# Optimization experiments

Hardware: AMD Instinct MI355X
Metric: run time of the kernel (lower is better)

## Reference

```python
import jax, jax.numpy as jnp
import numpy as np

N_NODES = 100000
N_PER_GRAPH = 200
N_GRAPHS = N_NODES // N_PER_GRAPH
N_EDGES = 400000
F_IN = 37
H = 128          # node_hidden == transformer_hidden == fc_hidden
HEADS = 8
K_SEEDS = 75     # ceil(0.25 * 300) -> PyG GMT defaults


def _lin(key, out_d, in_d):
    kw, kb = jax.random.split(key)
    w = jax.random.normal(kw, (out_d, in_d), jnp.float32) * float(1.0 / np.sqrt(in_d))
    b = jax.random.normal(kb, (out_d,), jnp.float32) * 0.02
    return w, b


def gcn_layer(x, W, b, src, dst, n):
    # PyG GCNConv with add_self_loops and symmetric deg^-1/2 normalization
    h = x @ W.T                                   # [n, out]
    deg = jnp.ones((n,), h.dtype).at[dst].add(1.0)   # in-degree + self loop
    dinv = jax.lax.rsqrt(deg)
    msg = h[src] * (dinv[src] * dinv[dst])[:, None]  # gather + edge normalize
    agg = jnp.zeros_like(h).at[dst].add(msg)         # scatter-add
    agg = agg + h * (dinv * dinv)[:, None]           # self-loop message
    return agg + b


def attn_block(Q, K, V, fo_W, fo_b):
    # MAB core of GMT: multi-head attention (scaled by sqrt(dim_V)) + rFF residual
    B, nq, d = Q.shape
    dh = d // HEADS
    Qh = Q.reshape(B, nq, HEADS, dh)
    Kh = K.reshape(B, K.shape[1], HEADS, dh)
    Vh = V.reshape(B, V.shape[1], HEADS, dh)
    scores = jnp.einsum('bqhd,bkhd->bhqk', Qh, Kh) / jnp.sqrt(jnp.asarray(d, Q.dtype))
    A = jax.nn.softmax(scores, axis=-1)
    O = jnp.einsum('bhqk,bkhd->bqhd', A, Vh).reshape(B, nq, d)
    out = Q + O
    return out + jax.nn.relu(out @ fo_W.T + fo_b)


def setup_inputs() -> dict:
    key = jax.random.key(0)
    k = iter(jax.random.split(key, 64))
    inp = {}
    inp['herg_em'] = jax.random.normal(next(k), (1, 1280), jnp.float32)
    inp['x'] = jax.random.normal(next(k), (N_NODES, F_IN), jnp.float32)
    inp['edge_attr'] = jax.random.normal(next(k), (N_EDGES, 4), jnp.float32)
    inp['mol_rep'] = jax.random.normal(next(k), (N_GRAPHS, 11), jnp.float32)
    for i, in_d in enumerate([F_IN, H, H, H]):
        inp[f'conv_W{i}'], inp[f'conv_b{i}'] = _lin(next(k), H, in_d)
    inp['lin1_W'], inp['lin1_b'] = _lin(next(k), H, H)
    inp['lin2_W'], inp['lin2_b'] = _lin(next(k), H, H)
    inp['S1'] = jax.random.normal(next(k), (1, K_SEEDS, H), jnp.float32) * 0.1
    for p in ['pma1', 'sab', 'pma2']:
        for nm in ['fq', 'k', 'v', 'fo']:
            inp[f'{p}_{nm}_W'], inp[f'{p}_{nm}_b'] = _lin(next(k), H, H)
    inp['S2'] = jax.random.normal(next(k), (1, 1, H), jnp.float32) * 0.1
    inp['herg_lin_W'], inp['herg_lin_b'] = _lin(next(k), H, 1280)
    inp['herg_out_W'], inp['herg_out_b'] = _lin(next(k), H, 2 * H)
    inp['fc0_W'], inp['fc0_b'] = _lin(next(k), H, H)
    inp['sig_W'], inp['sig_b'] = _lin(next(k), 1, H)
    inp['edge_index'] = jax.random.randint(next(k), (2, N_EDGES), 0, N_NODES, dtype=jnp.int32)
    inp['batch'] = jnp.arange(N_NODES, dtype=jnp.int32) // N_PER_GRAPH
    return inp


def reference(herg_em, x, edge_attr, mol_rep,
              conv_W0, conv_b0, conv_W1, conv_b1, conv_W2, conv_b2, conv_W3, conv_b3,
              lin1_W, lin1_b, lin2_W, lin2_b,
              S1, pma1_fq_W, pma1_fq_b, pma1_k_W, pma1_k_b, pma1_v_W, pma1_v_b, pma1_fo_W, pma1_fo_b,
              sab_fq_W, sab_fq_b, sab_k_W, sab_k_b, sab_v_W, sab_v_b, sab_fo_W, sab_fo_b,
              S2, pma2_fq_W, pma2_fq_b, pma2_k_W, pma2_k_b, pma2_v_W, pma2_v_b, pma2_fo_W, pma2_fo_b,
              herg_lin_W, herg_lin_b, herg_out_W, herg_out_b,
              fc0_W, fc0_b, sig_W, sig_b,
              edge_index, batch):
    src, dst = edge_index[0], edge_index[1]
    n = x.shape[0]

    # stacked GCNConv + ReLU
    h = jax.nn.relu(gcn_layer(x, conv_W0, conv_b0, src, dst, n))
    for W, b in ((conv_W1, conv_b1), (conv_W2, conv_b2), (conv_W3, conv_b3)):
        h = jax.nn.relu(gcn_layer(h, W, b, src, dst, n))

    # GraphMultisetTransformer: lin1 -> GMPool_G -> SelfAtt -> GMPool_I -> lin2
    hx = h @ lin1_W.T + lin1_b                     # [N, H]
    B = N_GRAPHS

    # GMPool_G: seeds attend to GCNConv-projected keys/values (dense per graph)
    Q = jnp.broadcast_to(S1, (B, K_SEEDS, H)) @ pma1_fq_W.T + pma1_fq_b
    K = gcn_layer(hx, pma1_k_W, pma1_k_b, src, dst, n).reshape(B, N_PER_GRAPH, H)
    V = gcn_layer(hx, pma1_v_W, pma1_v_b, src, dst, n).reshape(B, N_PER_GRAPH, H)
    xb = attn_block(Q, K, V, pma1_fo_W, pma1_fo_b)     # [B, 75, H]

    # SelfAtt (SAB)
    Q = xb @ sab_fq_W.T + sab_fq_b
    K = xb @ sab_k_W.T + sab_k_b
    V = xb @ sab_v_W.T + sab_v_b
    xb = attn_block(Q, K, V, sab_fo_W, sab_fo_b)       # [B, 75, H]

    # GMPool_I: single seed, Linear keys/values
    Q = jnp.broadcast_to(S2, (B, 1, H)) @ pma2_fq_W.T + pma2_fq_b
    K = xb @ pma2_k_W.T + pma2_k_b
    V = xb @ pma2_v_W.T + pma2_v_b
    xb = attn_block(Q, K, V, pma2_fo_W, pma2_fo_b)     # [B, 1, H]

    out = xb[:, 0, :] @ lin2_W.T + lin2_b              # [B, H]

    # hERG branch
    herg = jax.nn.relu(herg_em @ herg_lin_W.T + herg_lin_b)   # [1, 128]
    herg = jnp.broadcast_to(herg, (B, herg.shape[1]))
    out = jnp.concatenate([out, herg], axis=1)                 # [B, 256]
    out = jax.nn.relu(out @ herg_out_W.T + herg_out_b)
    out = jax.nn.relu(out @ fc0_W.T + fc0_b)                   # dropout = identity (eval)
    return jax.nn.sigmoid(out @ sig_W.T + sig_b)               # [B, 1]
```

## Files before the change

### kernel.cpp

```cpp
#include <hip/hip_runtime.h>
#include <hip/hip_bf16.h>

typedef unsigned short ushort_t;
typedef unsigned int uint_t;
typedef __attribute__((ext_vector_type(8))) short short8;
typedef __attribute__((ext_vector_type(4))) float float4v;

static constexpr int NN  = 100000;
static constexpr int NE  = 400000;
static constexpr int NB  = 500;
static constexpr int NS  = 75;
static constexpr int H   = 128;
static constexpr float SCALE = 0.08838834764831845f;

union U32 { uint_t u; float f; };
__device__ __forceinline__ float bf2f(ushort_t b){ U32 t; t.u = ((uint_t)b) << 16; return t.f; }
__device__ __forceinline__ ushort_t f2bf(float f){
    U32 t; t.f = f;
    uint_t r = t.u + 0x7fffu + ((t.u >> 16) & 1u);
    return (ushort_t)(r >> 16);
}
__device__ __forceinline__ void fma8(float* a, uint4 u, float c){
    a[0] += c * bf2f((ushort_t)(u.x & 0xffff)); a[1] += c * bf2f((ushort_t)(u.x >> 16));
    a[2] += c * bf2f((ushort_t)(u.y & 0xffff)); a[3] += c * bf2f((ushort_t)(u.y >> 16));
    a[4] += c * bf2f((ushort_t)(u.z & 0xffff)); a[5] += c * bf2f((ushort_t)(u.z >> 16));
    a[6] += c * bf2f((ushort_t)(u.w & 0xffff)); a[7] += c * bf2f((ushort_t)(u.w >> 16));
}

__global__ void k_hist(int* counts, const int* __restrict__ dst, int e){
    int i = blockIdx.x*256 + threadIdx.x;
    if (i < e) atomicAdd(&counts[dst[i]], 1);
}
__global__ __launch_bounds__(256) void k_scan1(const int* __restrict__ counts,
    int* __restrict__ row_start, int* __restrict__ blockSums,
    float* __restrict__ dinv, float* __restrict__ selfc, int n){
    __shared__ int s[256];
    int t = threadIdx.x, i = blockIdx.x*256 + t;
    int v = (i < n) ? counts[i] : 0;
    s[t] = v; __syncthreads();
    #pragma unroll
    for (int off = 1; off < 256; off <<= 1){
        int add = (t >= off) ? s[t-off] : 0;
        __syncthreads();
        s[t] += add;
        __syncthreads();
    }
    if (i < n){
        row_start[i] = s[t] - v;
        float r = rsqrtf(1.f + (float)v);
        dinv[i] = r; selfc[i] = r*r;
    }
    if (t == 255) blockSums[blockIdx.x] = s[255];
}
__global__ void k_scan3(int* __restrict__ row_start, int* __restrict__ cursor,
                        const int* __restrict__ blockOff, int n, int total){
    int i = blockIdx.x*256 + threadIdx.x;
    if (i < n){
        int v = row_start[i] + blockOff[i >> 8];
        row_start[i] = v; cursor[i] = v;
    }
    if (i == 0) row_start[n] = total;
}
__global__ void k_fillcsr(const int* __restrict__ src, const int* __restrict__ dst,
    const float* __restrict__ dinv, int* cursor,
    int* __restrict__ srcs_s, float* __restrict__ ce_s, int e){
    int i = blockIdx.x*256 + threadIdx.x;
    if (i < e){
        int d = dst[i], s = src[i];
        int p = atomicAdd(&cursor[d], 1);
        srcs_s[p] = s;
        ce_s[p] = dinv[s] * dinv[d];
    }
}

struct CvtArgs { const float* w[17]; const float* w0; const float* s1; const float* s2; const float* x37; };
static constexpr int CVT_W   = 17*16384;
static constexpr int CVT_W0  = 8192;
static constexpr int CVT_S1  = 9600;
static constexpr int CVT_S2  = 128;
static constexpr int CVT_X   = NN*64;
__global__ void k_cvt_all(CvtArgs a, ushort_t* __restrict__ wbf, ushort_t* __restrict__ w0bf,
                          ushort_t* __restrict__ s1bf, ushort_t* __restrict__ s2bf,
                          ushort_t* __restrict__ xb64, int* __restrict__ counts){
    int i = blockIdx.x*256 + threadIdx.x;
    if (i < NN) counts[i] = 0;
    if (i < CVT_W){ int idx = i >> 14, off = i & 16383; wbf[i] = f2bf(a.w[idx][off]); return; }
    i -= CVT_W;
    if (i < CVT_W0){ int r = i >> 6, c = i & 63; w0bf[i] = (c < 37) ? f2bf(a.w0[r*37 + c]) : (ushort_t)0; return; }
    i -= CVT_W0;
    if (i < CVT_S1){ s1bf[i] = f2bf(a.s1[i]); return; }
    i -= CVT_S1;
    if (i < CVT_S2){ s2bf[i] = f2bf(a.s2[i]); return; }
    i -= CVT_S2;
    if (i < CVT_X){ int r = i >> 6, c = i & 63; xb64[i] = (c < 37) ? f2bf(a.x37[(size_t)r*37 + c]) : (ushort_t)0; return; }
}

__global__ __launch_bounds__(512) void k_seedq_scan2(
    const ushort_t* __restrict__ s1bf, const ushort_t* __restrict__ s2bf,
    const ushort_t* __restrict__ W1, const float* __restrict__ bias1,
    const ushort_t* __restrict__ W2q, const float* __restrict__ bias2,
    ushort_t* __restrict__ q0, ushort_t* __restrict__ q2,
    const float* __restrict__ hem, const float* __restrict__ hlW,
    const float* __restrict__ hlb, float* __restrict__ hergv,
    const int* __restrict__ blockSums, int* __restrict__ blockOff, int nb)
{
    int blk = blockIdx.x;
    int tid  = threadIdx.x;
    if (blk == 4){
        __shared__ int s[512];
        int t = tid;
        int v = (t < nb) ? blockSums[t] : 0;
        s[t] = v; __syncthreads();
        #pragma unroll
        for (int off = 1; off < 512; off <<= 1){
            int add = (t >= off) ? s[t-off] : 0;
            __syncthreads();
            s[t] += add;
            __syncthreads();
        }
        blockOff[t] = s[t] - v;
        return;
    }
    if (blk == 3){
        __shared__ float e[1280];
        for (int i = tid; i < 1280; i += 512) e[i] = hem[i];
        __syncthreads();
        if (tid < 128){
            float acc = 0.f;
            for (int k = 0; k < 1280; ++k) acc += e[k] * hlW[(size_t)tid*1280 + k];
            hergv[tid] = fmaxf(acc + hlb[tid], 0.f);
        }
        return;
    }
    if (tid >= 256) return;
    const ushort_t* x = (blk < 2) ? s1bf : s2bf;
    const ushort_t* W = (blk < 2) ? W1 : W2q;
    const float* bias = (blk < 2) ? bias1 : bias2;
    ushort_t* out = (blk < 2) ? q0 : q2;
    int M = (blk < 2) ? NS : 1;
    int base = (blk < 2) ? blk*64 : 0;
    int wid  = tid >> 6;
    int lane = tid & 63;
    int l15  = lane & 15, quad = lane >> 4;
    int row0 = base + wid*16;
    int ar   = row0 + l15; if (ar > M-1) ar = M-1;
    const short* xr = (const short*)(x + (size_t)ar*H) + quad*8;
    float4v acc[8];
    #pragma unroll
    for (int i = 0; i < 8; ++i) acc[i] = (float4v)0.f;
    #pragma unroll
    for (int kc = 0; kc < 4; ++kc){
        short8 a = *(const short8*)(xr + kc*32);
        #pragma unroll
        for (int nt = 0; nt < 8; ++nt){
            short8 b = *(const short8*)((const short*)(W + (size_t)(nt*16 + l15)*H) + kc*32 + quad*8);
            acc[nt] = __builtin_amdgcn_mfma_f32_16x16x32_bf16(a, b, acc[nt], 0, 0, 0);
        }
    }
    #pragma unroll
    for (int nt = 0; nt < 8; ++nt){
        int c = nt*16 + l15;
        float bv = bias[c];
        #pragma unroll
        for (int reg = 0; reg < 4; ++reg){
            int r = row0 + quad*4 + reg;
            if (r >= M) continue;
            out[(size_t)r*H + c] = f2bf(acc[nt][reg] + bv);
        }
    }
}

template<int NOUT, int RELU, int STAGE2, int MINW>
__global__ __launch_bounds__(256, MINW) void k_conv_fused3(
    const ushort_t* __restrict__ x,
    const int* __restrict__ row_st, const int* __restrict__ srcs,
    const float* __restrict__ ces, const float* __restrict__ selfc,
    const ushort_t* __restrict__ W, const float* __restrict__ bias0,
    const float* __restrict__ bias1,
    const ushort_t* __restrict__ W2, const float* __restrict__ bias2,
    ushort_t* __restrict__ out0, ushort_t* __restrict__ out1)
{
    __shared__ ushort_t As[32][136];
    __shared__ ushort_t Bs[(NOUT==16)?32:1][(NOUT==16)?136:1];
    const int tid = threadIdx.x;
    const int node = tid >> 3, qq = tid & 7;
    const int g = blockIdx.x*32 + node;
    float acc[16];
    #pragma unroll
    for (int i = 0; i < 16; ++i) acc[i] = 0.f;
    if (g < NN){
        const uint4* xr = (const uint4*)(x + (size_t)g*H + qq*16);
        float sc = selfc[g];
        uint4 u0 = xr[0], u1 = xr[1];
        fma8(acc+0, u0, sc); fma8(acc+8, u1, sc);
        int e = row_st[g], e1 = row_st[g+1];
        int sA = 0, sB = 0; float cA = 0.f, cB = 0.f;
        if (e < e1){ sA = srcs[e]; cA = ces[e]; }
        if (e + 1 < e1){ sB = srcs[e+1]; cB = ces[e+1]; }
        while (e + 2 <= e1){
            int sA2 = 0, sB2 = 0; float cA2 = 0.f, cB2 = 0.f;
            if (e + 2 < e1){ sA2 = srcs[e+2]; cA2 = ces[e+2]; }
            if (e + 3 < e1){ sB2 = srcs[e+3]; cB2 = ces[e+3]; }
            const uint4* pa = (const uint4*)(x + (size_t)sA*H + qq*16);
            const uint4* pb = (const uint4*)(x + (size_t)sB*H + qq*16);
            uint4 a0 = pa[0], a1 = pa[1];
            uint4 c0 = pb[0], c1 = pb[1];
            fma8(acc+0, a0, cA); fma8(acc+8, a1, cA);
            fma8(acc+0, c0, cB); fma8(acc+8, c1, cB);
            sA = sA2; sB = sB2; cA = cA2; cB = cB2;
            e += 2;
        }
        if (e < e1){
            const uint4* pa = (const uint4*)(x + (size_t)sA*H + qq*16);
            uint4 a0 = pa[0], a1 = pa[1];
            fma8(acc+0, a0, cA); fma8(acc+8, a1, cA);
        }
    }
    {
        uint_t* dst = (uint_t*)&As[node][qq*16];
        #pragma unroll
        for (int i = 0; i < 8; ++i)
            dst[i] = (uint_t)f2bf(acc[2*i]) | ((uint_t)f2bf(acc[2*i+1]) << 16);
    }
    __syncthreads();
    const int w = tid >> 6, lane = tid & 63, l15 = lane & 15, quad = lane >> 4;
    const int rt = w & 1;
    constexpr int NT = NOUT/2;
    const int ct0 = (w >> 1) * NT;
    float4v o[NT];
    #pragma unroll
    for (int t = 0; t < NT; ++t) o[t] = (float4v)0.f;
    #pragma unroll
    for (int kc = 0; kc < 4; ++kc){
        short8 a = *(const short8*)(&As[rt*16 + l15][kc*32 + quad*8]);
        #pragma unroll
        for (int t = 0; t < NT; ++t){
            short8 bfr = *(const short8*)(W + (size_t)((ct0 + t)*16 + l15)*H + kc*32 + quad*8);
            o[t] = __builtin_amdgcn_mfma_f32_16x16x32_bf16(a, bfr, o[t], 0, 0, 0);
        }
    }
    __syncthreads();
    #pragma unroll
    for (int t = 0; t < NT; ++t){
        int cg = (ct0 + t)*16 + l15;
        #pragma unroll
        for (int r = 0; r < 4; ++r){
            float v;
            if (NOUT == 8 || cg < 128){
                v = o[t][r] + bias0[cg];
                if (RELU) v = fmaxf(v, 0.f);
                As[rt*16 + quad*4 + r][cg] = f2bf(v);
            } else {
                v = o[t][r] + bias1[cg - 128];
                if (RELU) v = fmaxf(v, 0.f);
                Bs[rt*16 + quad*4 + r][cg - 128] = f2bf(v);
            }
        }
    }
    __syncthreads();
    if (STAGE2){
        float4v o2[4];
        #pragma unroll
        for (int t = 0; t < 4; ++t) o2[t] = (float4v)0.f;
        const int ct2 = (w >> 1) * 4;
        #pragma unroll
        for (int kc = 0; kc < 4; ++kc){
            short8 a = *(const short8*)(&As[rt*16 + l15][kc*32 + quad*8]);
            #pragma unroll
            for (int t = 0; t < 4; ++t){
                short8 bfr = *(const short8*)(W2 + (size_t)((ct2 + t)*16 + l15)*H + kc*32 + quad*8);
                o2[t] = __builtin_amdgcn_mfma_f32_16x16x32_bf16(a, bfr, o2[t], 0, 0, 0);
            }
        }
        __syncthreads();
        #pragma unroll
        for (int t = 0; t < 4; ++t){
            int cg = (ct2 + t)*16 + l15;
            #pragma unroll
            for (int r = 0; r < 4; ++r)
                As[rt*16 + quad*4 + r][cg] = f2bf(o2[t][r] + bias2[cg]);
        }
        __syncthreads();
    }
    if (g < NN){
        if (NOUT == 16){
            size_t kb = ((size_t)(qq >> 1)*NN + (size_t)g)*32 + (size_t)(qq & 1)*16;
            ((uint4*)(out0 + kb))[0] = *(const uint4*)&As[node][qq*16];
            ((uint4*)(out0 + kb))[1] = *(const uint4*)&As[node][qq*16 + 8];
            ((uint4*)(out1 + kb))[0] = *(const uint4*)&Bs[node][qq*16];
            ((uint4*)(out1 + kb))[1] = *(const uint4*)&Bs[node][qq*16 + 8];
        } else {
            uint4* op = (uint4*)(out0 + (size_t)g*H + qq*16);
            const uint4* sp = (const uint4*)&As[node][qq*16];
            op[0] = sp[0]; op[1] = sp[1];
        }
    }
}

__global__ __launch_bounds__(256, 8) void k_conv0b(
    const ushort_t* __restrict__ x,
    const int* __restrict__ row_st, const int* __restrict__ srcs,
    const float* __restrict__ ces, const float* __restrict__ selfc,
    const ushort_t* __restrict__ W,
    const float* __restrict__ bias,
    ushort_t* __restrict__ out)
{
    __shared__ ushort_t As[32][136];
    const int tid = threadIdx.x;
    const int node = tid >> 3, qq = tid & 7;
    const int g = blockIdx.x*32 + node;
    float acc[8];
    #pragma unroll
    for (int i = 0; i < 8; ++i) acc[i] = 0.f;
    if (g < NN){
        const uint4* xr = (const uint4*)(x + (size_t)g*64 + qq*8);
        float sc = selfc[g];
        fma8(acc, xr[0], sc);
        int e = row_st[g], e1 = row_st[g+1];
        int sA = 0, sB = 0; float cA = 0.f, cB = 0.f;
        if (e < e1){ sA = srcs[e]; cA = ces[e]; }
        if (e + 1 < e1){ sB = srcs[e+1]; cB = ces[e+1]; }
        while (e + 2 <= e1){
            int sA2 = 0, sB2 = 0; float cA2 = 0.f, cB2 = 0.f;
            if (e + 2 < e1){ sA2 = srcs[e+2]; cA2 = ces[e+2]; }
            if (e + 3 < e1){ sB2 = srcs[e+3]; cB2 = ces[e+3]; }
            uint4 a0 = *(const uint4*)(x + (size_t)sA*64 + qq*8);
            uint4 c0 = *(const uint4*)(x + (size_t)sB*64 + qq*8);
            fma8(acc, a0, cA);
            fma8(acc, c0, cB);
            sA = sA2; sB = sB2; cA = cA2; cB = cB2;
            e += 2;
        }
        if (e < e1){
            uint4 a0 = *(const uint4*)(x + (size_t)sA*64 + qq*8);
            fma8(acc, a0, cA);
        }
    }
    {
        uint_t* dst = (uint_t*)&As[node][qq*8];
        #pragma unroll
        for (int i = 0; i < 4; ++i)
            dst[i] = (uint_t)f2bf(acc[2*i]) | ((uint_t)f2bf(acc[2*i+1]) << 16);
    }
    __syncthreads();
    const int w = tid >> 6, lane = tid & 63, l15 = lane & 15, quad = lane >> 4;
    const int rt = w & 1;
    const int ct0 = (w >> 1) * 4;
    float4v o[4];
    #pragma unroll
    for (int t = 0; t < 4; ++t) o[t] = (float4v)0.f;
    #pragma unroll
    for (int kc = 0; kc < 2; ++kc){
        short8 a = *(const short8*)(&As[rt*16 + l15][kc*32 + quad*8]);
        #pragma unroll
        for (int t = 0; t < 4; ++t){
            short8 bfr = *(const short8*)(W + (size_t)((ct0 + t)*16 + l15)*64 + kc*32 + quad*8);
            o[t] = __builtin_amdgcn_mfma_f32_16x16x32_bf16(a, bfr, o[t], 0, 0, 0);
        }
    }
    __syncthreads();
    #pragma unroll
    for (int t = 0; t < 4; ++t){
        int cg = (ct0 + t)*16 + l15;
        #pragma unroll
        for (int r = 0; r < 4; ++r)
            As[rt*16 + quad*4 + r][cg] = f2bf(fmaxf(o[t][r] + bias[cg], 0.f));
    }
    __syncthreads();
    if (g < NN){
        uint4* op = (uint4*)(out + (size_t)g*H + qq*16);
        const uint4* sp = (const uint4*)&As[node][qq*16];
        op[0] = sp[0]; op[1] = sp[1];
    }
}

struct TailArgs {
    const ushort_t* Khm; const ushort_t* Vhm;
    const ushort_t* q0;  const ushort_t* q2;
    const ushort_t* p1foW; const float* p1fob;
    const ushort_t* sfqW;  const float* sfqb;
    const ushort_t* skW;   const float* skb;
    const ushort_t* svW;   const float* svb;
    const ushort_t* sfoW;  const float* sfob;
    const ushort_t* p2kW;  const float* p2kb;
    const ushort_t* p2vW;  const float* p2vb;
    const ushort_t* p2foW; const float* p2fob;
    const ushort_t* lin2W; const float* lin2b;
    const float* hergv;
    const float* hoW; const float* hob;
    const float* fcW; const float* fcb;
    const float* sW;  const float* sb;
    float* outp;
};

__global__ __launch_bounds__(512, 4) void k_graph_tail(TailArgs a){
    __shared__ ushort_t bufA[83*136];
    __shared__ ushort_t bufB[80*136];
    __shared__ ushort_t bufC[80*136];
    __shared__ ushort_t vt4[64*104];
    const int b = blockIdx.x, tid = threadIdx.x;
    const int w = tid >> 6, lane = tid & 63, l15 = lane & 15, quad = lane >> 4;

    for (int i = tid; i < 2*16*32; i += 512){
        int hh2 = i >> 9, rr = (i >> 5) & 15, kk = 200 + (i & 31);
        bufC[(hh2*16 + rr)*232 + kk] = 0;
    }
    for (int hp = 0; hp < 4; ++hp){
        __syncthreads();
        const ushort_t* Kb = a.Khm + ((size_t)hp*NB + b)*(size_t)200*32;
        for (int idx = tid; idx < 200*8; idx += 512){
            int key = idx >> 3, p = idx & 7;
            int hh = p >> 2, dl = (p & 3)*4;
            const uint_t* src = (const uint_t*)(Kb + (size_t)key*32 + hh*16 + dl);
            uint_t* d = (uint_t*)&bufB[(hh*208 + key)*24 + dl];
            d[0] = src[0]; d[1] = src[1];
        }
        const ushort_t* Vb = a.Vhm + ((size_t)hp*NB + b)*(size_t)200*32;
        for (int idx = tid; idx < 200*8; idx += 512){
            int key = idx >> 3, p = idx & 7;
            int hh = p >> 2, dl = (p & 3)*4;
            const ushort_t* src = Vb + (size_t)key*32 + hh*16 + dl;
            bufC[(hh*16 + dl+0)*232 + key] = src[0];
            bufC[(hh*16 + dl+1)*232 + key] = src[1];
            bufC[(hh*16 + dl+2)*232 + key] = src[2];
            bufC[(hh*16 + dl+3)*232 + key] = src[3];
        }
        __syncthreads();
        for (int j = w; j < 10; j += 8){
            int hl = j / 5, qt = j % 5;
            int gh = hp*2 + hl;
            ushort_t* psw = vt4 + w*512;
            int qr = qt*16 + l15; if (qr > NS-1) qr = NS-1;
            short8 av = *(const short8*)(a.q0 + (size_t)qr*H + gh*16 + (quad & 1)*8);
            short8 zero8 = (short8)0;
            bool klow = (quad < 2);
            short8 afrag = klow ? av : zero8;
            float4v s[13];
            #pragma unroll
            for (int kt = 0; kt < 13; ++kt){
                short8 bv = *(const short8*)(&bufB[(hl*208 + kt*16 + l15)*24 + (quad & 1)*8]);
                short8 bfrag = klow ? bv : zero8;
                s[kt] = __builtin_amdgcn_mfma_f32_16x16x32_bf16(afrag, bfrag, (float4v)0.f, 0, 0, 0);
            }
            float mx[4] = {-1e30f, -1e30f, -1e30f, -1e30f};
            #pragma unroll
            for (int kt = 0; kt < 13; ++kt){
                if (kt*16 + l15 >= 200){ s[kt][0]=-1e30f; s[kt][1]=-1e30f; s[kt][2]=-1e30f; s[kt][3]=-1e30f; }
                #pragma unroll
                for (int r = 0; r < 4; ++r) mx[r] = fmaxf(mx[r], s[kt][r]);
            }
            #pragma unroll
            for (int off = 1; off < 16; off <<= 1){
                #pragma unroll
                for (int r = 0; r < 4; ++r) mx[r] = fmaxf(mx[r], __shfl_xor(mx[r], off));
            }
            float sum[4] = {0.f, 0.f, 0.f, 0.f};
            float4v o = (float4v)0.f;
            #pragma unroll
            for (int kc = 0; kc < 7; ++kc){
                #pragma unroll
                for (int t2 = 0; t2 < 2; ++t2){
                    int kt = kc*2 + t2;
                    #pragma unroll
                    for (int r = 0; r < 4; ++r){
                        float e = 0.f;
                        if (kt < 13){ e = __expf((s[kt][r] - mx[r]) * SCALE); sum[r] += e; }
                        psw[(quad*4 + r)*32 + t2*16 + l15] = f2bf(e);
                    }
                }
                short8 pa = *(const short8*)(psw + l15*32 + quad*8);
                short8 vb = *(const short8*)(&bufC[(hl*16 + l15)*232 + kc*32 + quad*8]);
                o = __builtin_amdgcn_mfma_f32_16x16x32_bf16(pa, vb, o, 0, 0, 0);
            }
            #pragma unroll
            for (int off = 1; off < 16; off <<= 1){
                #pragma unroll
                for (int r = 0; r < 4; ++r) sum[r] += __shfl_xor(sum[r], off);
            }
            #pragma unroll
            for (int r = 0; r < 4; ++r){
                int row = qt*16 + quad*4 + r;
                if (row < NS){
                    float qv = bf2f(a.q0[(size_t)row*H + gh*16 + l15]);
                    bufA[row*136 + gh*16 + l15] = f2bf(qv + o[r] / sum[r]);
                }
            }
        }
    }
    __syncthreads();

    if (w >= 5){
        for (int i = tid - 320; i < 64*104/2; i += 192) ((uint_t*)vt4)[i] = 0u;
    }
    for (int rt = w; rt < 5; rt += 8){
        float4v o[8];
        #pragma unroll
        for (int i = 0; i < 8; ++i) o[i] = (float4v)0.f;
        #pragma unroll
        for (int kc = 0; kc < 4; ++kc){
            short8 av = *(const short8*)(bufA + (rt*16 + l15)*136 + kc*32 + quad*8);
            #pragma unroll
            for (int ct = 0; ct < 8; ++ct){
                short8 bv = *(const short8*)((const short*)(a.p1foW + (size_t)(ct*16 + l15)*H) + kc*32 + quad*8);
                o[ct] = __builtin_amdgcn_mfma_f32_16x16x32_bf16(av, bv, o[ct], 0, 0, 0);
            }
        }
        #pragma unroll
        for (int ct = 0; ct < 8; ++ct){
            int c = ct*16 + l15; float bb = a.p1fob[c];
            #pragma unroll
            for (int r = 0; r < 4; ++r){
                int row = rt*16 + quad*4 + r;
                float res = bf2f(bufA[row*136 + c]);
                bufA[row*136 + c] = f2bf(fmaxf(o[ct][r] + bb, 0.f) + res);
            }
        }
    }
    __syncthreads();

    for (int job = w; job < 40; job += 8){
        int rt = job >> 3, ct = job & 7;
        float4v o = (float4v)0.f;
        #pragma unroll
        for (int kc = 0; kc < 4; ++kc){
            short8 av = *(const short8*)(bufA + (rt*16 + l15)*136 + kc*32 + quad*8);
            short8 bv = *(const short8*)((const short*)(a.sfqW + (size_t)(ct*16 + l15)*H) + kc*32 + quad*8);
            o = __builtin_amdgcn_mfma_f32_16x16x32_bf16(av, bv, o, 0, 0, 0);
        }
        int c = ct*16 + l15; float bb = a.sfqb[c];
        #pragma unroll
        for (int r = 0; r < 4; ++r)
            bufB[(rt*16 + quad*4 + r)*136 + c] = f2bf(o[r] + bb);
    }
    for (int job = w; job < 40; job += 8){
        int rt = job >> 3, ct = job & 7;
        float4v o = (float4v)0.f;
        #pragma unroll
        for (int kc = 0; kc < 4; ++kc){
            short8 av = *(const short8*)(bufA + (rt*16 + l15)*136 + kc*32 + quad*8);
            short8 bv = *(const short8*)((const short*)(a.skW + (size_t)(ct*16 + l15)*H) + kc*32 + quad*8);
            o = __builtin_amdgcn_mfma_f32_16x16x32_bf16(av, bv, o, 0, 0, 0);
        }
        int c = ct*16 + l15; float bb = a.skb[c];
        #pragma unroll
        for (int r = 0; r < 4; ++r)
            bufC[(rt*16 + quad*4 + r)*136 + c] = f2bf(o[r] + bb);
    }
    __syncthreads();

    for (int pass = 0; pass < 2; ++pass){
        int hbase = pass*4;
        for (int job = w; job < 20; job += 8){
            int rt = job >> 2, ctl = job & 3;
            int ct = hbase + ctl;
            float4v o = (float4v)0.f;
            #pragma unroll
            for (int kc = 0; kc < 4; ++kc){
                short8 av = *(const short8*)(bufA + (rt*16 + l15)*136 + kc*32 + quad*8);
                short8 bv = *(const short8*)((const short*)(a.svW + (size_t)(ct*16 + l15)*H) + kc*32 + quad*8);
                o = __builtin_amdgcn_mfma_f32_16x16x32_bf16(av, bv, o, 0, 0, 0);
            }
            int c = ct*16 + l15; float bb = a.svb[c];
            #pragma unroll
            for (int r = 0; r < 4; ++r){
                int key = rt*16 + quad*4 + r;
                if (key < NS) vt4[(ctl*16 + l15)*104 + key] = f2bf(o[r] + bb);
            }
        }
        __syncthreads();
        if (w < 4){
            ushort_t* psw = (w == 0) ? bufA + 10200 :
                            (w == 1) ? bufA + 10712 :
                            (w == 2) ? bufB + 10200 : bufC + 10200;
            int hl = w, h = hbase + w;
            short8 zero8 = (short8)0;
            bool klow = (quad < 2);
            for (int qt = 0; qt < 5; ++qt){
                short8 av = *(const short8*)(bufB + (qt*16 + l15)*136 + h*16 + (quad & 1)*8);
                short8 afrag = klow ? av : zero8;
                float4v s[5];
                #pragma unroll
                for (int kt = 0; kt < 5; ++kt){
                    short8 bv = *(const short8*)(bufC + (kt*16 + l15)*136 + h*16 + (quad & 1)*8);
                    short8 bfrag = klow ? bv : zero8;
                    s[kt] = __builtin_amdgcn_mfma_f32_16x16x32_bf16(afrag, bfrag, (float4v)0.f, 0, 0, 0);
                }
                float mx[4] = {-1e30f, -1e30f, -1e30f, -1e30f};
                #pragma unroll
                for (int kt = 0; kt < 5; ++kt){
                    if (kt*16 + l15 >= NS){ s[kt][0]=-1e30f; s[kt][1]=-1e30f; s[kt][2]=-1e30f; s[kt][3]=-1e30f; }
                    #pragma unroll
                    for (int r = 0; r < 4; ++r) mx[r] = fmaxf(mx[r], s[kt][r]);
                }
                #pragma unroll
                for (int off = 1; off < 16; off <<= 1){
                    #pragma unroll
                    for (int r = 0; r < 4; ++r) mx[r] = fmaxf(mx[r], __shfl_xor(mx[r], off));
                }
                float sum[4] = {0.f, 0.f, 0.f, 0.f};
                float4v o = (float4v)0.f;
                #pragma unroll
                for (int kc = 0; kc < 3; ++kc){
                    #pragma unroll
                    for (int t2 = 0; t2 < 2; ++t2){
                        int kt = kc*2 + t2;
                        #pragma unroll
                        for (int r = 0; r < 4; ++r){
                            float e = 0.f;
                            if (kt < 5){ e = __expf((s[kt][r] - mx[r]) * SCALE); sum[r] += e; }
                            psw[(quad*4 + r)*32 + t2*16 + l15] = f2bf(e);
                        }
                    }
                    short8 pa = *(const short8*)(psw + l15*32 + quad*8);
                    short8 vb = *(const short8*)(vt4 + (hl*16 + l15)*104 + kc*32 + quad*8);
                    o = __builtin_amdgcn_mfma_f32_16x16x32_bf16(pa, vb, o, 0, 0, 0);
                }
                #pragma unroll
                for (int off = 1; off < 16; off <<= 1){
                    #pragma unroll
                    for (int r = 0; r < 4; ++r) sum[r] += __shfl_xor(sum[r], off);
                }
                #pragma unroll
                for (int r = 0; r < 4; ++r){
                    int row = qt*16 + quad*4 + r;
                    if (row < NS){
                        float qv = bf2f(bufB[row*136 + h*16 + l15]);
                        bufB[row*136 + h*16 + l15] = f2bf(qv + o[r] / sum[r]);
                    }
                }
            }
        }
        __syncthreads();
    }

    for (int job = w; job < 40; job += 8){
        int rt = job >> 3, ct = job & 7;
        float4v o = (float4v)0.f;
        #pragma unroll
        for (int kc = 0; kc < 4; ++kc){
            short8 av = *(const short8*)(bufB + (rt*16 + l15)*136 + kc*32 + quad*8);
            short8 bv = *(const short8*)((const short*)(a.sfoW + (size_t)(ct*16 + l15)*H) + kc*32 + quad*8);
            o = __builtin_amdgcn_mfma_f32_16x16x32_bf16(av, bv, o, 0, 0, 0);
        }
        int c = ct*16 + l15; float bb = a.sfob[c];
        #pragma unroll
        for (int r = 0; r < 4; ++r){
            int row = rt*16 + quad*4 + r;
            bufA[row*136 + c] = f2bf(fmaxf(o[r] + bb, 0.f) + bf2f(bufB[row*136 + c]));
        }
    }
    __syncthreads();

    for (int job = w; job < 40; job += 8){
        int rt = job >> 3, ct = job & 7;
        float4v o = (float4v)0.f;
        #pragma unroll
        for (int kc = 0; kc < 4; ++kc){
            short8 av = *(const short8*)(bufA + (rt*16 + l15)*136 + kc*32 + quad*8);
            short8 bv = *(const short8*)((const short*)(a.p2kW + (size_t)(ct*16 + l15)*H) + kc*32 + quad*8);
            o = __builtin_amdgcn_mfma_f32_16x16x32_bf16(av, bv, o, 0, 0, 0);
        }
        int c = ct*16 + l15; float bb = a.p2kb[c];
        #pragma unroll
        for (int r = 0; r < 4; ++r)
            bufC[(rt*16 + quad*4 + r)*136 + c] = f2bf(o[r] + bb);
    }
    for (int job = w; job < 40; job += 8){
        int rt = job >> 3, ct = job & 7;
        float4v o = (float4v)0.f;
        #pragma unroll
        for (int kc = 0; kc < 4; ++kc){
            short8 av = *(const short8*)(bufA + (rt*16 + l15)*136 + kc*32 + quad*8);
            short8 bv = *(const short8*)((const short*)(a.p2vW + (size_t)(ct*16 + l15)*H) + kc*32 + quad*8);
            o = __builtin_amdgcn_mfma_f32_16x16x32_bf16(av, bv, o, 0, 0, 0);
        }
        int c = ct*16 + l15; float bb = a.p2vb[c];
        #pragma unroll
        for (int r = 0; r < 4; ++r)
            bufB[(rt*16 + quad*4 + r)*136 + c] = f2bf(o[r] + bb);
    }
    __syncthreads();

    {
        int t = tid;
        char* sb8 = (char*)bufA;
        float* sc       = (float*)sb8;
        float* sumh     = (float*)(sb8 + 2432);
        ushort_t* xa    = (ushort_t*)(sb8 + 2464);
        ushort_t* xb3   = (ushort_t*)(sb8 + 2720);
        float* tt       = (float*)(sb8 + 2976);
        float* v256     = (float*)(sb8 + 3488);
        float* red      = (float*)(sb8 + 4512);
        if (t < 256){
            int h = t >> 5, l32 = t & 31;
            const ushort_t* qr = a.q2 + h*16;
            for (int k = l32; k < NS; k += 32){
                float s = 0.f;
                #pragma unroll
                for (int d = 0; d < 16; ++d) s += bf2f(qr[d]) * bf2f(bufC[k*136 + h*16 + d]);
                sc[h*76 + k] = s;
            }
        }
        __syncthreads();
        if (t < 128){
            int hh = t >> 4, i = t & 15;
            float mx = -1e30f;
            for (int k = i; k < NS; k += 16) mx = fmaxf(mx, sc[hh*76 + k]);
            #pragma unroll
            for (int off = 1; off < 16; off <<= 1) mx = fmaxf(mx, __shfl_xor(mx, off));
            float sm = 0.f;
            for (int k = i; k < NS; k += 16){
                float e = __expf((sc[hh*76 + k] - mx) * SCALE);
                sc[hh*76 + k] = e;
                sm += e;
            }
            #pragma unroll
            for (int off = 1; off < 16; off <<= 1) sm += __shfl_xor(sm, off);
            if (i == 0) sumh[hh] = sm;
        }
        __syncthreads();
        if (t < 128){
            int hh = t >> 4;
            float o = 0.f;
            for (int k = 0; k < NS; ++k) o += sc[hh*76 + k] * bf2f(bufB[k*136 + t]);
            xa[t] = f2bf(bf2f(a.q2[t]) + o / sumh[hh]);
        }
        __syncthreads();
        if (t < 128){
            float acc = 0.f;
            const ushort_t* wr = a.p2foW + (size_t)t*H;
            for (int k = 0; k < H; ++k) acc += bf2f(xa[k]) * bf2f(wr[k]);
            xb3[t] = f2bf(fmaxf(acc + a.p2fob[t], 0.f) + bf2f(xa[t]));
        }
        __syncthreads();
        if (t < 128){
            float acc = 0.f;
            const ushort_t* wr = a.lin2W + (size_t)t*H;
            for (int k = 0; k < H; ++k) acc += bf2f(xb3[k]) * bf2f(wr[k]);
            v256[t] = acc + a.lin2b[t];
            v256[128 + t] = a.hergv[t];
        }
        __syncthreads();
        if (t < 128){
            float acc = 0.f;
            const float* wr = a.hoW + (size_t)t*256;
            for (int k = 0; k < 256; ++k) acc += v256[k] * wr[k];
            tt[t] = fmaxf(acc + a.hob[t], 0.f);
        }
        __syncthreads();
        if (t < 128){
            float acc = 0.f;
            const float* wr = a.fcW + (size_t)t*128;
            for (int k = 0; k < 128; ++k) acc += tt[k] * wr[k];
            float uv = fmaxf(acc + a.fcb[t], 0.f);
            red[t] = uv * a.sW[t];
        }
        __syncthreads();
        for (int s = 64; s > 0; s >>= 1){
            if (t < s) red[t] += red[t + s];
            __syncthreads();
        }
        if (t == 0){
            float logit = red[0] + a.sb[0];
            a.outp[b] = 1.f / (1.f + expf(-logit));
        }
    }
}

extern "C" void kernel_launch(void* const* d_in, const int* in_sizes, int n_in,
                              void* d_out, int out_size, void* d_ws, size_t ws_size,
                              hipStream_t stream)
{
    (void)in_sizes; (void)n_in; (void)out_size; (void)ws_size;
    const float* herg_em = (const float*)d_in[0];
    const float* x_in    = (const float*)d_in[1];
    const float* convW[4] = {(const float*)d_in[4], (const float*)d_in[6], (const float*)d_in[8], (const float*)d_in[10]};
    const float* convB[4] = {(const float*)d_in[5], (const float*)d_in[7], (const float*)d_in[9], (const float*)d_in[11]};
    const float* lin1W = (const float*)d_in[12]; const float* lin1b = (const float*)d_in[13];
    const float* lin2W = (const float*)d_in[14]; const float* lin2b = (const float*)d_in[15];
    const float* S1    = (const float*)d_in[16];
    const float* p1fqW = (const float*)d_in[17]; const float* p1fqb = (const float*)d_in[18];
    const float* p1kW  = (const float*)d_in[19]; const float* p1kb  = (const float*)d_in[20];
    const float* p1vW  = (const float*)d_in[21]; const float* p1vb  = (const float*)d_in[22];
    const float* p1foW = (const float*)d_in[23]; const float* p1fob = (const float*)d_in[24];
    const float* sfqW  = (const float*)d_in[25]; const float* sfqb  = (const float*)d_in[26];
    const float* skW   = (const float*)d_in[27]; const float* skb   = (const float*)d_in[28];
    const float* svW   = (const float*)d_in[29]; const float* svb   = (const float*)d_in[30];
    const float* sfoW  = (const float*)d_in[31]; const float* sfob  = (const float*)d_in[32];
    const float* p2fqW = (const float*)d_in[33]; const float* p2fqb = (const float*)d_in[34];
    const float* p2kW  = (const float*)d_in[35]; const float* p2kb  = (const float*)d_in[36];
    const float* p2vW  = (const float*)d_in[37]; const float* p2vb  = (const float*)d_in[38];
    const float* p2foW = (const float*)d_in[39]; const float* p2fob = (const float*)d_in[40];
    const float* S2    = (const float*)d_in[41];
    const float* hlW   = (const float*)d_in[42]; const float* hlb   = (const float*)d_in[43];
    const float* hoW   = (const float*)d_in[44]; const float* hob   = (const float*)d_in[45];
    const float* fcW   = (const float*)d_in[46]; const float* fcb   = (const float*)d_in[47];
    const float* sW    = (const float*)d_in[48]; const float* sb    = (const float*)d_in[49];
    const int*  ei    = (const int*)d_in[50];
    const int*  esrc  = ei;
    const int*  edst  = ei + NE;
    float* outp = (float*)d_out;

    char* WS = (char*)d_ws;
    int*   counts = (int*)(WS + 0);
    int*   cursor = (int*)(WS + 400384);
    int*   row_st = (int*)(WS + 800768);
    int*   bSums  = (int*)(WS + 1201152);
    int*   bOff   = (int*)(WS + 1203200);
    float* dinv   = (float*)(WS + 1205248);
    float* selfc  = (float*)(WS + 1605632);
    int*   srcs_s = (int*)(WS + 2005632);
    float* ce_s   = (float*)(WS + 3605632);
    ushort_t* wbf = (ushort_t*)(WS + 5205632);
    ushort_t* w0bf= (ushort_t*)(WS + 5762688);
    ushort_t* s1bf= (ushort_t*)(WS + 5779072);
    ushort_t* s2bf= (ushort_t*)(WS + 5798272);
    ushort_t* q0  = (ushort_t*)(WS + 5798528);
    ushort_t* q2  = (ushort_t*)(WS + 5817728);
    float* hergv  = (float*)(WS + 5817984);
    ushort_t* xb64= (ushort_t*)(WS + 6074496);
    ushort_t* b0  = (ushort_t*)(WS + 18874496);
    ushort_t* b1  = (ushort_t*)(WS + 44474496);
    ushort_t* b2  = (ushort_t*)(WS + 70074496);

    const int gN   = (NN + 255)/256;
    const int gE   = (NE + 255)/256;
    const int gC   = (NN + 31)/32;

    CvtArgs ca;
    ca.w[0]=convW[1]; ca.w[1]=convW[2]; ca.w[2]=convW[3]; ca.w[3]=lin1W; ca.w[4]=lin2W;
    ca.w[5]=p1kW; ca.w[6]=p1vW; ca.w[7]=p1foW;
    ca.w[8]=sfqW; ca.w[9]=skW; ca.w[10]=svW; ca.w[11]=sfoW;
    ca.w[12]=p2kW; ca.w[13]=p2vW; ca.w[14]=p2foW; ca.w[15]=p1fqW; ca.w[16]=p2fqW;
    ca.w0 = convW[0]; ca.s1 = S1; ca.s2 = S2; ca.x37 = x_in;
    const int cvtTotal = CVT_W + CVT_W0 + CVT_S1 + CVT_S2 + CVT_X;
    k_cvt_all<<<(cvtTotal + 255)/256, 256, 0, stream>>>(ca, wbf, w0bf, s1bf, s2bf, xb64, counts);

    k_hist  <<<gE, 256, 0, stream>>>(counts, edst, NE);
    k_scan1 <<<gN, 256, 0, stream>>>(counts, row_st, bSums, dinv, selfc, NN);
    k_seedq_scan2<<<5, 512, 0, stream>>>(s1bf, s2bf, wbf + (size_t)15*16384, p1fqb,
                                   wbf + (size_t)16*16384, p2fqb, q0, q2,
                                   herg_em, hlW, hlb, hergv,
                                   bSums, bOff, gN);
    k_scan3 <<<gN, 256, 0, stream>>>(row_st, cursor, bOff, NN, NE);
    k_fillcsr<<<gE, 256, 0, stream>>>(esrc, edst, dinv, cursor, srcs_s, ce_s, NE);

    k_conv0b<<<gC, 256, 0, stream>>>(xb64, row_st, srcs_s, ce_s, selfc, w0bf, convB[0], b0);
    k_conv_fused3<8,1,0,8><<<gC, 256, 0, stream>>>(b0, row_st, srcs_s, ce_s, selfc,
        wbf + (size_t)0*16384, convB[1], nullptr, nullptr, nullptr, b1, nullptr);
    k_conv_fused3<8,1,0,8><<<gC, 256, 0, stream>>>(b1, row_st, srcs_s, ce_s, selfc,
        wbf + (size_t)1*16384, convB[2], nullptr, nullptr, nullptr, b0, nullptr);
    k_conv_fused3<8,1,1,8><<<gC, 256, 0, stream>>>(b0, row_st, srcs_s, ce_s, selfc,
        wbf + (size_t)2*16384, convB[3], nullptr, wbf + (size_t)3*16384, lin1b, b1, nullptr);
    k_conv_fused3<16,0,0,4><<<gC, 256, 0, stream>>>(b1, row_st, srcs_s, ce_s, selfc,
        wbf + (size_t)5*16384, p1kb, p1vb, nullptr, nullptr, b2, b0);

    TailArgs ta;
    ta.Khm = b2; ta.Vhm = b0; ta.q0 = q0; ta.q2 = q2;
    ta.p1foW = wbf + (size_t)7*16384;  ta.p1fob = p1fob;
    ta.sfqW  = wbf + (size_t)8*16384;  ta.sfqb  = sfqb;
    ta.skW   = wbf + (size_t)9*16384;  ta.skb   = skb;
    ta.svW   = wbf + (size_t)10*16384; ta.svb   = svb;
    ta.sfoW  = wbf + (size_t)11*16384; ta.sfob  = sfob;
    ta.p2kW  = wbf + (size_t)12*16384; ta.p2kb  = p2kb;
    ta.p2vW  = wbf + (size_t)13*16384; ta.p2vb  = p2vb;
    ta.p2foW = wbf + (size_t)14*16384; ta.p2fob = p2fob;
    ta.lin2W = wbf + (size_t)4*16384;  ta.lin2b = lin2b;
    ta.hergv = hergv;
    ta.hoW = hoW; ta.hob = hob;
    ta.fcW = fcW; ta.fcb = fcb;
    ta.sW = sW; ta.sb = sb;
    ta.outp = outp;
    k_graph_tail<<<NB, 512, 0, stream>>>(ta);
}
```

Baseline: 642.8 us.

## Process four heads per stage in PMA1 attention and read K directly from global

The PMA1 attention stage in the graph tail kernel now stages V for four heads per iteration instead of two, halving the outer loop count and its block barriers, and spreads 20 work items over 8 waves instead of 10. K tiles are no longer copied into shared memory. MFMA B fragments are loaded straight from global memory with clamped key indices. The P scratch moves into bufB and vt4 grows to hold the extra V heads. This trades shared-memory staging and syncs for more global or L2 traffic on K reads, and raises shared memory per block.

```diff
diff --git a/kernel.cpp b/kernel.cpp
--- a/kernel.cpp
+++ b/kernel.cpp
@@ -394,42 +394,42 @@
 };
 
 __global__ __launch_bounds__(512, 4) void k_graph_tail(TailArgs a){
-    __shared__ ushort_t bufA[83*136];
+    __shared__ ushort_t bufA[85*136];
     __shared__ ushort_t bufB[80*136];
     __shared__ ushort_t bufC[80*136];
-    __shared__ ushort_t vt4[64*104];
+    __shared__ ushort_t vt4[7424];
     const int b = blockIdx.x, tid = threadIdx.x;
     const int w = tid >> 6, lane = tid & 63, l15 = lane & 15, quad = lane >> 4;
 
-    for (int i = tid; i < 2*16*32; i += 512){
-        int hh2 = i >> 9, rr = (i >> 5) & 15, kk = 200 + (i & 31);
-        bufC[(hh2*16 + rr)*232 + kk] = 0;
-    }
-    for (int hp = 0; hp < 4; ++hp){
-        __syncthreads();
-        const ushort_t* Kb = a.Khm + ((size_t)hp*NB + b)*(size_t)200*32;
-        for (int idx = tid; idx < 200*8; idx += 512){
-            int key = idx >> 3, p = idx & 7;
+    for (int i = tid; i < 64*32; i += 512){
+        int r4 = i >> 5, kk = 200 + (i & 31);
+        int head4 = r4 >> 4, dim = r4 & 15;
+        ushort_t* dst = (head4 < 2) ? &bufC[(head4*16 + dim)*232] : &vt4[((head4-2)*16 + dim)*232];
+        dst[kk] = 0;
+    }
+    for (int hpp = 0; hpp < 2; ++hpp){
+        __syncthreads();
+        for (int idx = tid; idx < 2*200*8; idx += 512){
+            int hpl = idx / 1600, rem = idx % 1600;
+            int key = rem >> 3, p = rem & 7;
             int hh = p >> 2, dl = (p & 3)*4;
-            const uint_t* src = (const uint_t*)(Kb + (size_t)key*32 + hh*16 + dl);
-            uint_t* d = (uint_t*)&bufB[(hh*208 + key)*24 + dl];
-            d[0] = src[0]; d[1] = src[1];
-        }
-        const ushort_t* Vb = a.Vhm + ((size_t)hp*NB + b)*(size_t)200*32;
-        for (int idx = tid; idx < 200*8; idx += 512){
-            int key = idx >> 3, p = idx & 7;
-            int hh = p >> 2, dl = (p & 3)*4;
-            const ushort_t* src = Vb + (size_t)key*32 + hh*16 + dl;
-            bufC[(hh*16 + dl+0)*232 + key] = src[0];
-            bufC[(hh*16 + dl+1)*232 + key] = src[1];
-            bufC[(hh*16 + dl+2)*232 + key] = src[2];
-            bufC[(hh*16 + dl+3)*232 + key] = src[3];
-        }
-        __syncthreads();
-        for (int j = w; j < 10; j += 8){
-            int hl = j / 5, qt = j % 5;
-            int gh = hp*2 + hl;
-            ushort_t* psw = vt4 + w*512;
+            int hp = hpp*2 + hpl;
+            int head4 = hpl*2 + hh;
+            const ushort_t* src = a.Vhm + ((size_t)hp*NB + b)*(size_t)200*32 + (size_t)key*32 + hh*16 + dl;
+            ushort_t* base = (head4 < 2) ? &bufC[(head4*16)*232] : &vt4[((head4-2)*16)*232];
+            base[(dl+0)*232 + key] = src[0];
+            base[(dl+1)*232 + key] = src[1];
+            base[(dl+2)*232 + key] = src[2];
+            base[(dl+3)*232 + key] = src[3];
+        }
+        __syncthreads();
+        for (int j = w; j < 20; j += 8){
+            int hl4 = j / 5, qt = j % 5;
+            int hp = hpp*2 + (hl4 >> 1);
+            int hh = hl4 & 1;
+            int gh = hp*2 + hh;
+            ushort_t* psw = bufB + w*512;
+            const ushort_t* Kb = a.Khm + ((size_t)hp*NB + b)*(size_t)200*32;
             int qr = qt*16 + l15; if (qr > NS-1) qr = NS-1;
             short8 av = *(const short8*)(a.q0 + (size_t)qr*H + gh*16 + (quad & 1)*8);
             short8 zero8 = (short8)0;
@@ -438,7 +438,8 @@
             float4v s[13];
             #pragma unroll
             for (int kt = 0; kt < 13; ++kt){
-                short8 bv = *(const short8*)(&bufB[(hl*208 + kt*16 + l15)*24 + (quad & 1)*8]);
+                int kk = kt*16 + l15; if (kk > 199) kk = 199;
+                short8 bv = *(const short8*)(Kb + (size_t)kk*32 + hh*16 + (quad & 1)*8);
                 short8 bfrag = klow ? bv : zero8;
                 s[kt] = __builtin_amdgcn_mfma_f32_16x16x32_bf16(afrag, bfrag, (float4v)0.f, 0, 0, 0);
             }
@@ -454,6 +455,7 @@
                 #pragma unroll
                 for (int r = 0; r < 4; ++r) mx[r] = fmaxf(mx[r], __shfl_xor(mx[r], off));
             }
+            const ushort_t* vbase = (hl4 < 2) ? &bufC[(hl4*16)*232] : &vt4[((hl4-2)*16)*232];
             float sum[4] = {0.f, 0.f, 0.f, 0.f};
             float4v o = (float4v)0.f;
             #pragma unroll
@@ -469,7 +471,7 @@
                     }
                 }
                 short8 pa = *(const short8*)(psw + l15*32 + quad*8);
-                short8 vb = *(const short8*)(&bufC[(hl*16 + l15)*232 + kc*32 + quad*8]);
+                short8 vb = *(const short8*)(vbase + l15*232 + kc*32 + quad*8);
                 o = __builtin_amdgcn_mfma_f32_16x16x32_bf16(pa, vb, o, 0, 0, 0);
             }
             #pragma unroll
```

Measured after the change: 628.9 us. -2.2%, faster.
